# Kernel tuning notes

Hardware: AMD Instinct MI355X
Metric: run time of the kernel (lower is better)

The kernel has to match this reference:

```python
import jax, jax.numpy as jnp
import numpy as np
from jax.ops import segment_max, segment_sum

N_NODES = 50000
N_EDGES = 800000
IN_CH = 256
HEADS = 8
OUT_CH = 32
NEG_SLOPE = 0.2
EPS = 1e-16


def setup_inputs() -> dict:
    key = jax.random.key(0)
    k1, k2, k3, k4, k5 = jax.random.split(key, 5)
    x = jax.random.normal(k1, (N_NODES, IN_CH), dtype=jnp.float32)
    edge_index = jax.random.randint(k2, (2, N_EDGES), 0, N_NODES, dtype=jnp.int64)
    # params (xavier-ish scale)
    W = jax.random.normal(k3, (HEADS * OUT_CH, IN_CH), dtype=jnp.float32) * (1.0 / np.sqrt(IN_CH))
    a_left = jax.random.normal(k4, (HEADS, OUT_CH), dtype=jnp.float32) * (1.0 / np.sqrt(OUT_CH))
    a_right = jax.random.normal(k5, (HEADS, OUT_CH), dtype=jnp.float32) * (1.0 / np.sqrt(OUT_CH))
    return {"x": x, "edge_index": edge_index, "W": W, "a_left": a_left, "a_right": a_right}


def reference(x, edge_index, W, a_left, a_right):
    N = x.shape[0]
    H, C = HEADS, OUT_CH
    # add self loops
    loops = jnp.arange(N, dtype=edge_index.dtype)
    src = jnp.concatenate([edge_index[0], loops])
    dst = jnp.concatenate([edge_index[1], loops])
    # Wh: [N, H, C]
    Wh = (x @ W.T).reshape(N, H, C)
    # per-node attention halves: [N, H]
    e_left = jnp.einsum('nhc,hc->nh', Wh, a_left)
    e_right = jnp.einsum('nhc,hc->nh', Wh, a_right)
    # per-edge score: [E, H]
    e = e_left[src] + e_right[dst]
    e = jnp.where(e >= 0, e, NEG_SLOPE * e)
    # segment softmax over edges grouped by dst
    e_max = segment_max(e, dst, num_segments=N)
    e_max = jnp.where(jnp.isfinite(e_max), e_max, 0.0)
    e_exp = jnp.exp(e - e_max[dst])
    denom = segment_sum(e_exp, dst, num_segments=N)
    alpha = e_exp / (denom[dst] + EPS)
    # scatter-add aggregation: [N, H, C]
    out = segment_sum(Wh[src] * alpha[:, :, None], dst, num_segments=N)
    return out.reshape(N, H * C)
```

## Files before the change

### kernel.cpp

```cpp
#include <hip/hip_runtime.h>
#include <hip/hip_bf16.h>

#define N_NODES 50000
#define N_EDGES 800000
#define IN_CH 256
#define HEADS 8
#define OUT_CH 32
#define HC 256
#define E_TOT (N_EDGES + N_NODES)
#define NEG_SLOPE 0.2f

typedef short s16x8 __attribute__((ext_vector_type(8)));
typedef float f32x4 __attribute__((ext_vector_type(4)));

__device__ __forceinline__ unsigned short f2bf(float f) {
    unsigned int u = __float_as_uint(f);
    unsigned int r = (u + 0x7FFFu + ((u >> 16) & 1u)) >> 16;
    return (unsigned short)r;
}
__device__ __forceinline__ float bf2f(unsigned short b) {
    return __uint_as_float(((unsigned int)b) << 16);
}

__device__ __forceinline__ int tbyte(int r, int k2) { return (r * 64 + k2) ^ ((r & 7) << 4); }

__global__ void wconv_kernel(const float* __restrict__ W, unsigned short* __restrict__ Wb) {
    int i = (blockIdx.x * 256 + threadIdx.x) * 4;
    float4 v = *(const float4*)&W[i];
    ushort4 o; o.x = f2bf(v.x); o.y = f2bf(v.y); o.z = f2bf(v.z); o.w = f2bf(v.w);
    *(ushort4*)&Wb[i] = o;
}

__global__ __launch_bounds__(512) void gemm_kernel(const float* __restrict__ x,
                                                   const unsigned short* __restrict__ Wb,
                                                   const float* __restrict__ a_left,
                                                   const float* __restrict__ a_right,
                                                   unsigned short* __restrict__ Wh,
                                                   float* __restrict__ el,
                                                   float* __restrict__ er) {
    __shared__ unsigned short As[128 * 32];
    __shared__ unsigned short Bs[256 * 32];
    char* Asb = (char*)As;
    char* Bsb = (char*)Bs;
    const int m0 = blockIdx.x * 128;
    const int t  = threadIdx.x;
    const int l  = t & 63;
    const int wv = t >> 6;
    const int wr = wv & 3;
    const int wc = wv >> 2;
    const int c16  = l & 15;
    const int rgrp = l >> 4;

    f32x4 acc[2][8];
#pragma unroll
    for (int i = 0; i < 2; ++i)
#pragma unroll
        for (int j = 0; j < 8; ++j) acc[i][j] = (f32x4){0.f, 0.f, 0.f, 0.f};

    for (int k0 = 0; k0 < IN_CH; k0 += 32) {
        {
            int r = t >> 2, kq = (t & 3) << 3;
            float4 v0 = make_float4(0.f, 0.f, 0.f, 0.f), v1 = v0;
            if (m0 + r < N_NODES) {
                const float* xp = &x[(size_t)(m0 + r) * IN_CH + k0 + kq];
                v0 = *(const float4*)(xp + 0);
                v1 = *(const float4*)(xp + 4);
            }
            ushort4 o0, o1;
            o0.x = f2bf(v0.x); o0.y = f2bf(v0.y); o0.z = f2bf(v0.z); o0.w = f2bf(v0.w);
            o1.x = f2bf(v1.x); o1.y = f2bf(v1.y); o1.z = f2bf(v1.z); o1.w = f2bf(v1.w);
            int b0 = kq * 2;
            *(ushort4*)(Asb + tbyte(r, b0 + 0)) = o0;
            *(ushort4*)(Asb + tbyte(r, b0 + 8)) = o1;
        }
        {
            int r = t >> 1, kq = (t & 1) << 4;
            const unsigned short* wp = &Wb[(size_t)r * IN_CH + k0 + kq];
            ushort4 w0 = *(const ushort4*)(wp + 0);
            ushort4 w1 = *(const ushort4*)(wp + 4);
            ushort4 w2 = *(const ushort4*)(wp + 8);
            ushort4 w3 = *(const ushort4*)(wp + 12);
            int b0 = kq * 2;
            *(ushort4*)(Bsb + tbyte(r, b0 + 0))  = w0;
            *(ushort4*)(Bsb + tbyte(r, b0 + 8))  = w1;
            *(ushort4*)(Bsb + tbyte(r, b0 + 16)) = w2;
            *(ushort4*)(Bsb + tbyte(r, b0 + 24)) = w3;
        }
        __syncthreads();
        s16x8 af0 = *(const s16x8*)(Asb + tbyte(wr * 32 + c16,      rgrp * 16));
        s16x8 af1 = *(const s16x8*)(Asb + tbyte(wr * 32 + 16 + c16, rgrp * 16));
#pragma unroll
        for (int nt = 0; nt < 8; ++nt) {
            s16x8 bf = *(const s16x8*)(Bsb + tbyte(wc * 128 + nt * 16 + c16, rgrp * 16));
            acc[0][nt] = __builtin_amdgcn_mfma_f32_16x16x32_bf16(af0, bf, acc[0][nt], 0, 0, 0);
            acc[1][nt] = __builtin_amdgcn_mfma_f32_16x16x32_bf16(af1, bf, acc[1][nt], 0, 0, 0);
        }
        __syncthreads();
    }

#pragma unroll
    for (int mt = 0; mt < 2; ++mt) {
#pragma unroll
        for (int hp = 0; hp < 4; ++hp) {
            int hg  = wc * 4 + hp;
            int nt0 = hp * 2;
            float al0 = a_left [hg * OUT_CH + c16];
            float al1 = a_left [hg * OUT_CH + 16 + c16];
            float ar0 = a_right[hg * OUT_CH + c16];
            float ar1 = a_right[hg * OUT_CH + 16 + c16];
#pragma unroll
            for (int rg = 0; rg < 4; ++rg) {
                float pl = acc[mt][nt0][rg] * al0 + acc[mt][nt0 + 1][rg] * al1;
                float pr = acc[mt][nt0][rg] * ar0 + acc[mt][nt0 + 1][rg] * ar1;
#pragma unroll
                for (int m = 1; m < 16; m <<= 1) {
                    pl += __shfl_xor(pl, m, 16);
                    pr += __shfl_xor(pr, m, 16);
                }
                int row = m0 + wr * 32 + mt * 16 + rgrp * 4 + rg;
                if (c16 == 0 && row < N_NODES) {
                    el[row * HEADS + hg] = pl;
                    er[row * HEADS + hg] = pr;
                }
            }
        }
#pragma unroll
        for (int nt = 0; nt < 8; ++nt) {
#pragma unroll
            for (int rg = 0; rg < 4; ++rg) {
                int row = m0 + wr * 32 + mt * 16 + rgrp * 4 + rg;
                if (row < N_NODES)
                    Wh[(size_t)row * HC + wc * 128 + nt * 16 + c16] = f2bf(acc[mt][nt][rg]);
            }
        }
    }
}

__global__ void zero_kernel(int* __restrict__ p, int n) {
    int i = blockIdx.x * blockDim.x + threadIdx.x;
    if (i < n) p[i] = 0;
}

__global__ void hist_kernel(const int* __restrict__ src, const int* __restrict__ dst,
                            int* __restrict__ count) {
    int e = blockIdx.x * blockDim.x + threadIdx.x;
    if (e >= E_TOT) return;
    int s, d;
    if (e < N_EDGES) { s = src[e]; d = dst[e]; } else { s = d = e - N_EDGES; }
    if ((unsigned)s >= N_NODES || (unsigned)d >= N_NODES) return;
    atomicAdd(&count[d], 1);
}

__global__ __launch_bounds__(1024) void scan_kernel(const int* __restrict__ count,
                                                    int* __restrict__ offset,
                                                    int* __restrict__ cursor) {
    __shared__ int wtot[16];
    __shared__ int wbase[16];
    __shared__ int running_s;
    int t = threadIdx.x, lane = t & 63, wid = t >> 6;
    if (t == 0) running_s = 0;
    __syncthreads();
    for (int base = 0; base < N_NODES; base += 1024) {
        int idx = base + t;
        int v = (idx < N_NODES) ? count[idx] : 0;
        int s = v;
#pragma unroll
        for (int off = 1; off < 64; off <<= 1) {
            int u = __shfl_up(s, off, 64);
            if (lane >= off) s += u;
        }
        if (lane == 63) wtot[wid] = s;
        __syncthreads();
        if (t == 0) {
            int b = running_s;
            for (int w = 0; w < 16; ++w) { wbase[w] = b; b += wtot[w]; }
            running_s = b;
        }
        __syncthreads();
        int excl = s - v + wbase[wid];
        if (idx < N_NODES) { offset[idx] = excl; cursor[idx] = excl; }
        __syncthreads();
    }
    if (t == 0) offset[N_NODES] = running_s;
}

__global__ void scatter_kernel(const int* __restrict__ src, const int* __restrict__ dst,
                               int* __restrict__ cursor, int* __restrict__ srcs) {
    int e = blockIdx.x * blockDim.x + threadIdx.x;
    if (e >= E_TOT) return;
    int s, d;
    if (e < N_EDGES) { s = src[e]; d = dst[e]; } else { s = d = e - N_EDGES; }
    if ((unsigned)s >= N_NODES || (unsigned)d >= N_NODES) return;
    int pos = atomicAdd(&cursor[d], 1);
    srcs[pos] = s;
}

__global__ __launch_bounds__(256) void agg_kernel(const unsigned short* __restrict__ Wh,
                                                  const float* __restrict__ el,
                                                  const float* __restrict__ er,
                                                  const int* __restrict__ offset,
                                                  const int* __restrict__ srcs,
                                                  float* __restrict__ out) {
    __shared__ float e_sh[64][HEADS];
    __shared__ int   s_sh[64];
    int n = blockIdx.x;
    int t = threadIdx.x;
    int h = t >> 5;
    int l32 = t & 31;
    float ern = er[n * HEADS + h];
    int start = offset[n], end = offset[n + 1];
    float acc = 0.f, denp = 0.f;

    for (int c0 = start; c0 < end; c0 += 64) {
        int m = min(64, end - c0);
#pragma unroll 2
        for (int jj = l32; jj < m; jj += 32) {
            int s = srcs[c0 + jj];
            if (h == 0) s_sh[jj] = s;
            float sc = el[s * HEADS + h] + ern;
            sc = fmaxf(sc, NEG_SLOPE * sc);
            float e = __expf(sc);
            e_sh[jj][h] = e;
            denp += e;
        }
        __syncthreads();
#pragma unroll 4
        for (int jj = 0; jj < m; ++jj) {
            int s   = s_sh[jj];
            float e = e_sh[jj][h];
            acc = fmaf(e, bf2f(Wh[(size_t)s * HC + t]), acc);
        }
        __syncthreads();
    }
#pragma unroll
    for (int m = 16; m >= 1; m >>= 1) denp += __shfl_xor(denp, m);
    out[(size_t)n * HC + t] = acc / (denp + 1e-16f);
}

__global__ void sentinel_kernel(float* __restrict__ out, int n) {
    int i = blockIdx.x * blockDim.x + threadIdx.x;
    if (i < n) out[i] = 1.0e6f;
}

extern "C" void kernel_launch(void* const* d_in, const int* in_sizes, int n_in,
                              void* d_out, int out_size, void* d_ws, size_t ws_size,
                              hipStream_t stream) {
    const float* x       = (const float*)d_in[0];
    const int*   ei      = (const int*)d_in[1];
    const float* W       = (const float*)d_in[2];
    const float* a_left  = (const float*)d_in[3];
    const float* a_right = (const float*)d_in[4];
    float* out = (float*)d_out;

    const int* src = ei;
    const int* dst = ei + N_EDGES;

    char* ws = (char*)d_ws;
    size_t off = 0;
    auto alloc = [&](size_t bytes) -> void* {
        void* p = ws + off;
        off += (bytes + 255) & ~(size_t)255;
        return p;
    };
    unsigned short* Wh = (unsigned short*)alloc((size_t)N_NODES * HC * sizeof(unsigned short));
    float* el     = (float*)alloc((size_t)N_NODES * HEADS * sizeof(float));
    float* er     = (float*)alloc((size_t)N_NODES * HEADS * sizeof(float));
    int*   count  = (int*)alloc((size_t)N_NODES * sizeof(int));
    int*   offset = (int*)alloc((size_t)(N_NODES + 1) * sizeof(int));
    int*   cursor = (int*)alloc((size_t)N_NODES * sizeof(int));
    int*   srcs   = (int*)alloc((size_t)E_TOT * sizeof(int));
    unsigned short* Wb = (unsigned short*)alloc((size_t)HC * IN_CH * sizeof(unsigned short));

    if (off > ws_size) {
        sentinel_kernel<<<(out_size + 255) / 256, 256, 0, stream>>>(out, out_size);
        return;
    }

    wconv_kernel<<<(HC * IN_CH) / 1024, 256, 0, stream>>>(W, Wb);
    gemm_kernel<<<(N_NODES + 127) / 128, 512, 0, stream>>>(x, Wb, a_left, a_right, Wh, el, er);

    zero_kernel<<<(N_NODES + 255) / 256, 256, 0, stream>>>(count, N_NODES);
    int eblocks = (E_TOT + 255) / 256;
    hist_kernel<<<eblocks, 256, 0, stream>>>(src, dst, count);
    scan_kernel<<<1, 1024, 0, stream>>>(count, offset, cursor);
    scatter_kernel<<<eblocks, 256, 0, stream>>>(src, dst, cursor, srcs);

    agg_kernel<<<N_NODES, 256, 0, stream>>>(Wh, el, er, offset, srcs, out);
}
```

Before: 368.0 us.

## Parallelize the offset scan and map one wavefront per node in aggregation

The single-block serial scan over all nodes is replaced by a three-kernel scan: per-block partial scans, a scan of block totals, then an apply pass. This removes a long serialized launch from the critical path. The aggregation kernel now gives each node one 64-lane wavefront instead of a 256-thread block. It passes source indices and exp scores through lane shuffles instead of shared memory and barriers, and loads 4 bf16 values per lane. The scan now hardcodes the final offset as the full edge count, which assumes every edge index is valid.

```diff
diff --git a/kernel.cpp b/kernel.cpp
--- a/kernel.cpp
+++ b/kernel.cpp
@@ -9,6 +9,7 @@
 #define HC 256
 #define E_TOT (N_EDGES + N_NODES)
 #define NEG_SLOPE 0.2f
+#define NB 196
 
 typedef short s16x8 __attribute__((ext_vector_type(8)));
 typedef float f32x4 __attribute__((ext_vector_type(4)));
@@ -151,37 +152,61 @@
     atomicAdd(&count[d], 1);
 }
 
-__global__ __launch_bounds__(1024) void scan_kernel(const int* __restrict__ count,
-                                                    int* __restrict__ offset,
-                                                    int* __restrict__ cursor) {
-    __shared__ int wtot[16];
-    __shared__ int wbase[16];
-    __shared__ int running_s;
+__global__ __launch_bounds__(256) void scan_part(const int* __restrict__ count,
+                                                 int* __restrict__ loc,
+                                                 int* __restrict__ btot) {
+    __shared__ int wt[4], wb[4];
     int t = threadIdx.x, lane = t & 63, wid = t >> 6;
-    if (t == 0) running_s = 0;
+    int idx = blockIdx.x * 256 + t;
+    int v = (idx < N_NODES) ? count[idx] : 0;
+    int s = v;
+#pragma unroll
+    for (int off = 1; off < 64; off <<= 1) {
+        int u = __shfl_up(s, off, 64);
+        if (lane >= off) s += u;
+    }
+    if (lane == 63) wt[wid] = s;
     __syncthreads();
-    for (int base = 0; base < N_NODES; base += 1024) {
-        int idx = base + t;
-        int v = (idx < N_NODES) ? count[idx] : 0;
-        int s = v;
-#pragma unroll
-        for (int off = 1; off < 64; off <<= 1) {
-            int u = __shfl_up(s, off, 64);
-            if (lane >= off) s += u;
-        }
-        if (lane == 63) wtot[wid] = s;
-        __syncthreads();
-        if (t == 0) {
-            int b = running_s;
-            for (int w = 0; w < 16; ++w) { wbase[w] = b; b += wtot[w]; }
-            running_s = b;
-        }
-        __syncthreads();
-        int excl = s - v + wbase[wid];
-        if (idx < N_NODES) { offset[idx] = excl; cursor[idx] = excl; }
-        __syncthreads();
-    }
-    if (t == 0) offset[N_NODES] = running_s;
+    if (t == 0) {
+        int a = 0;
+        for (int w = 0; w < 4; ++w) { wb[w] = a; a += wt[w]; }
+        btot[blockIdx.x] = a;
+    }
+    __syncthreads();
+    if (idx < N_NODES) loc[idx] = s - v + wb[wid];
+}
+
+__global__ __launch_bounds__(256) void scan_tops(const int* __restrict__ btot,
+                                                 int* __restrict__ bbase) {
+    __shared__ int wt[4], wb[4];
+    int t = threadIdx.x, lane = t & 63, wid = t >> 6;
+    int v = (t < NB) ? btot[t] : 0;
+    int s = v;
+#pragma unroll
+    for (int off = 1; off < 64; off <<= 1) {
+        int u = __shfl_up(s, off, 64);
+        if (lane >= off) s += u;
+    }
+    if (lane == 63) wt[wid] = s;
+    __syncthreads();
+    if (t == 0) {
+        int a = 0;
+        for (int w = 0; w < 4; ++w) { wb[w] = a; a += wt[w]; }
+    }
+    __syncthreads();
+    if (t < NB) bbase[t] = s - v + wb[wid];
+}
+
+__global__ __launch_bounds__(256) void scan_apply(int* __restrict__ offset,
+                                                  const int* __restrict__ bbase,
+                                                  int* __restrict__ cursor) {
+    int idx = blockIdx.x * 256 + threadIdx.x;
+    if (idx == 0) offset[N_NODES] = E_TOT;
+    if (idx < N_NODES) {
+        int o = offset[idx] + bbase[blockIdx.x];
+        offset[idx] = o;
+        cursor[idx] = o;
+    }
 }
 
 __global__ void scatter_kernel(const int* __restrict__ src, const int* __restrict__ dst,
@@ -195,46 +220,61 @@
     srcs[pos] = s;
 }
 
-__global__ __launch_bounds__(256) void agg_kernel(const unsigned short* __restrict__ Wh,
+__global__ __launch_bounds__(128) void agg_kernel(const unsigned short* __restrict__ Wh,
                                                   const float* __restrict__ el,
                                                   const float* __restrict__ er,
                                                   const int* __restrict__ offset,
                                                   const int* __restrict__ srcs,
                                                   float* __restrict__ out) {
-    __shared__ float e_sh[64][HEADS];
-    __shared__ int   s_sh[64];
-    int n = blockIdx.x;
-    int t = threadIdx.x;
-    int h = t >> 5;
-    int l32 = t & 31;
+    int n = blockIdx.x * 2 + (threadIdx.x >> 6);
+    if (n >= N_NODES) return;
+    int l = threadIdx.x & 63;
+    int h = l >> 3;
+    int i = l & 7;
     float ern = er[n * HEADS + h];
     int start = offset[n], end = offset[n + 1];
-    float acc = 0.f, denp = 0.f;
+    f32x4 acc = {0.f, 0.f, 0.f, 0.f};
+    float den = 0.f;
 
     for (int c0 = start; c0 < end; c0 += 64) {
-        int m = min(64, end - c0);
-#pragma unroll 2
-        for (int jj = l32; jj < m; jj += 32) {
-            int s = srcs[c0 + jj];
-            if (h == 0) s_sh[jj] = s;
+        int m = end - c0; if (m > 64) m = 64;
+        int sv = (l < m) ? srcs[c0 + l] : 0;
+
+        float e[8];
+#pragma unroll
+        for (int k = 0; k < 8; ++k) {
+            if (8 * k >= m) break;
+            int jj = i + 8 * k;
+            int s = __shfl(sv, jj, 64);
             float sc = el[s * HEADS + h] + ern;
             sc = fmaxf(sc, NEG_SLOPE * sc);
-            float e = __expf(sc);
-            e_sh[jj][h] = e;
-            denp += e;
-        }
-        __syncthreads();
-#pragma unroll 4
-        for (int jj = 0; jj < m; ++jj) {
-            int s   = s_sh[jj];
-            float e = e_sh[jj][h];
-            acc = fmaf(e, bf2f(Wh[(size_t)s * HC + t]), acc);
-        }
-        __syncthreads();
-    }
-#pragma unroll
-    for (int m = 16; m >= 1; m >>= 1) denp += __shfl_xor(denp, m);
-    out[(size_t)n * HC + t] = acc / (denp + 1e-16f);
+            float ev = (jj < m) ? __expf(sc) : 0.f;
+            e[k] = ev;
+            den += ev;
+        }
+
+#pragma unroll
+        for (int k = 0; k < 8; ++k) {
+            if (8 * k >= m) break;
+#pragma unroll
+            for (int q = 0; q < 8; ++q) {
+                int jj = k * 8 + q;
+                if (jj >= m) break;
+                float ev = __shfl(e[k], h * 8 + q, 64);
+                int   s  = __shfl(sv, jj, 64);
+                ushort4 w = *(const ushort4*)&Wh[(size_t)s * HC + h * 32 + i * 4];
+                acc.x = fmaf(ev, bf2f(w.x), acc.x);
+                acc.y = fmaf(ev, bf2f(w.y), acc.y);
+                acc.z = fmaf(ev, bf2f(w.z), acc.z);
+                acc.w = fmaf(ev, bf2f(w.w), acc.w);
+            }
+        }
+    }
+#pragma unroll
+    for (int msk = 4; msk >= 1; msk >>= 1) den += __shfl_xor(den, msk, 64);
+    float inv = 1.0f / (den + 1e-16f);
+    float4 o = make_float4(acc.x * inv, acc.y * inv, acc.z * inv, acc.w * inv);
+    *(float4*)&out[(size_t)n * HC + h * 32 + i * 4] = o;
 }
 
 __global__ void sentinel_kernel(float* __restrict__ out, int n) {
@@ -270,6 +310,8 @@
     int*   cursor = (int*)alloc((size_t)N_NODES * sizeof(int));
     int*   srcs   = (int*)alloc((size_t)E_TOT * sizeof(int));
     unsigned short* Wb = (unsigned short*)alloc((size_t)HC * IN_CH * sizeof(unsigned short));
+    int*   btot   = (int*)alloc((size_t)NB * sizeof(int));
+    int*   bbase  = (int*)alloc((size_t)NB * sizeof(int));
 
     if (off > ws_size) {
         sentinel_kernel<<<(out_size + 255) / 256, 256, 0, stream>>>(out, out_size);
@@ -282,8 +324,10 @@
     zero_kernel<<<(N_NODES + 255) / 256, 256, 0, stream>>>(count, N_NODES);
     int eblocks = (E_TOT + 255) / 256;
     hist_kernel<<<eblocks, 256, 0, stream>>>(src, dst, count);
-    scan_kernel<<<1, 1024, 0, stream>>>(count, offset, cursor);
+    scan_part<<<NB, 256, 0, stream>>>(count, offset, btot);
+    scan_tops<<<1, 256, 0, stream>>>(btot, bbase);
+    scan_apply<<<NB, 256, 0, stream>>>(offset, bbase, cursor);
     scatter_kernel<<<eblocks, 256, 0, stream>>>(src, dst, cursor, srcs);
 
-    agg_kernel<<<N_NODES, 256, 0, stream>>>(Wh, el, er, offset, srcs, out);
-}
+    agg_kernel<<<(N_NODES + 1) / 2, 128, 0, stream>>>(Wh, el, er, offset, srcs, out);
+}
```

After: 326.4 us. -11.3%, faster.
